# Performance work log

Measured on AMD Instinct MI355X. Metric: run time of the kernel, lower is better.

The kernel has to match this reference:

```python
import jax, jax.numpy as jnp
import numpy as np

N, D, C = 16384, 64, 128
MARGIN = 1.0
EPS_NORM = 1e-6   # F.normalize eps
EPS_PD = 1e-6     # F.pairwise_distance eps (added to the difference elementwise)


def setup_inputs() -> dict:
    key = jax.random.key(0)
    embeddings = jax.random.normal(key, (N, D), dtype=jnp.float32)
    labels = (jnp.arange(N) % C).astype(jnp.int32).reshape(N, 1)
    # deterministic valid positive: same label (i % C), different index
    pos_idx = ((jnp.arange(N) + C) % N).astype(jnp.int32)
    return {"embeddings": embeddings, "labels": labels, "pos_idx": pos_idx}


def reference(embeddings, labels, pos_idx):
    # L2-normalize rows (torch F.normalize: x / max(||x||, eps))
    nrm = jnp.linalg.norm(embeddings, axis=1, keepdims=True)
    e = embeddings / jnp.maximum(nrm, EPS_NORM)

    lab = labels[:, 0]
    # torch pairwise_distance computes ||x1 - x2 + eps||_2, eps added per element:
    # ||xi - xj + eps||^2 = ||xi||^2 + ||xj||^2 - 2 xi.xj + 2*eps*(sum(xi)-sum(xj)) + D*eps^2
    sq = jnp.sum(e * e, axis=1)          # [N]
    s = jnp.sum(e, axis=1)               # [N]
    gram = e @ e.T                        # [N, N]
    d2 = (sq[:, None] + sq[None, :] - 2.0 * gram
          + 2.0 * EPS_PD * (s[:, None] - s[None, :]) + D * EPS_PD * EPS_PD)
    d2 = jnp.maximum(d2, 0.0)
    dist = jnp.sqrt(jnp.maximum(d2, 1e-12))  # guard sqrt grad at 0

    # one positive per anchor: squared distance
    pos_loss = jnp.sum(d2[jnp.arange(N), pos_idx])

    # all negatives per anchor: hinge^2 on (margin - dist)
    neg_mask = lab[:, None] != lab[None, :]
    hinge = jnp.maximum(MARGIN - dist, 0.0)
    neg_loss = jnp.sum(jnp.where(neg_mask, hinge * hinge, 0.0))

    n_comparisons = N + jnp.sum(neg_mask)
    return (pos_loss + neg_loss) / n_comparisons.astype(jnp.float32)
```

## Files before the change

### kernel.cpp

```cpp
#include <hip/hip_runtime.h>
#include <hip/hip_bf16.h>

#define NN 16384
#define DD 64
#define NBI 32
#define NUNITS 2112
#define NBLK 512
#define NPOSB (NN/4)
#define SCREEN_T 0.49f

constexpr float F_EPS_PD   = 1e-6f;
constexpr float F_EPS_NORM = 1e-6f;

using bf16x8 = __attribute__((ext_vector_type(8))) short;
using f32x4  = __attribute__((ext_vector_type(4))) float;
typedef __attribute__((address_space(1))) const unsigned int gu32_t;
typedef __attribute__((address_space(3))) unsigned int       lu32_t;

__device__ __forceinline__ float wave_sum_f(float v) {
    #pragma unroll
    for (int o = 32; o >= 1; o >>= 1) v += __shfl_xor(v, o);
    return v;
}

__device__ __forceinline__ int band_off(int I) { return 2 * I * (65 - I); }

__global__ __launch_bounds__(256) void norm_kernel(
    const float* __restrict__ emb, const int* __restrict__ pidx,
    const int* __restrict__ lab, float2* __restrict__ up,
    float2* __restrict__ vcp, __hip_bfloat16* __restrict__ ebf,
    float* __restrict__ posP) {
    int w    = threadIdx.x >> 6;
    int row  = blockIdx.x * 4 + w;
    int lane = threadIdx.x & 63;
    int j    = pidx[row];
    float x  = emb[(size_t)row * DD + lane];
    float xj = emb[(size_t)j   * DD + lane];

    float n2  = wave_sum_f(x * x);
    float sx  = wave_sum_f(x);
    float n2j = wave_sum_f(xj * xj);
    float sxj = wave_sum_f(xj);
    float dot = wave_sum_f(x * xj);

    float m  = fmaxf(sqrtf(n2),  F_EPS_NORM);
    float mj = fmaxf(sqrtf(n2j), F_EPS_NORM);
    ebf[(size_t)row * DD + lane] = __float2bfloat16(x / m);

    __shared__ float spos[4];
    if (lane == 0) {
        float sq  = n2 / (m * m);
        float sqj = n2j / (mj * mj);
        float s   = sx / m;
        float sj  = sxj / mj;
        float g   = dot / (m * mj);
        float lf  = (float)lab[row];
        up[row]  = make_float2(sq + 2.0f * F_EPS_PD * s, lf);
        vcp[row] = make_float2(
            sq - 2.0f * F_EPS_PD * s + (float)DD * F_EPS_PD * F_EPS_PD, lf);
        float d2p = sq + sqj - 2.0f * g + 2.0f * F_EPS_PD * (s - sj)
                  + (float)DD * F_EPS_PD * F_EPS_PD;
        spos[w] = fmaxf(d2p, 0.0f);
    }
    __syncthreads();
    if (threadIdx.x == 0)
        posP[blockIdx.x] = spos[0] + spos[1] + spos[2] + spos[3];
}

__device__ __forceinline__ void stage_tile(const short* ebf, const float2* vcp,
                                           int tile, short* slotB, float2* slotV,
                                           int w, int lane) {
    const short* tbase = ebf + (size_t)tile * (128 * DD);
    int rlo = lane >> 3;
    int g   = (lane & 7) ^ rlo;
    #pragma unroll
    for (int q = 0; q < 2; ++q) {
        int m = w * 2 + q;
        __builtin_amdgcn_global_load_lds(
            (gu32_t*)(const void*)(tbase + (size_t)(8 * m + rlo) * DD + g * 8),
            (lu32_t*)(void*)(slotB + m * 512), 16, 0, 0);
    }
    __builtin_amdgcn_global_load_lds(
        (gu32_t*)(const void*)(vcp + (size_t)tile * 128 + lane * 2),
        (lu32_t*)(void*)slotV, 16, 0, 0);
}

__global__ __launch_bounds__(512, 4) void pair_kernel(
    const short* __restrict__ ebf, const float2* __restrict__ up,
    const float2* __restrict__ vcp, float* __restrict__ negP) {
    __shared__ short  ringB[3][8192];
    __shared__ float2 ringV[3][128];
    __shared__ float2 uband[512];
    __shared__ float  sred[8];
    int tid  = threadIdx.x;
    int w    = tid >> 6;
    int lane = tid & 63;
    int lrow = lane & 15, lkh = lane >> 4;
    int c0s  = ((lkh)     ^ (lrow & 7)) * 8;
    int c1s  = ((lkh + 4) ^ (lrow & 7)) * 8;

    int ks = (int)(((long long)blockIdx.x * NUNITS) / NBLK);
    int ke = (int)(((long long)(blockIdx.x + 1) * NUNITS) / NBLK);

    int I = (int)((65.0f - sqrtf(4225.0f - 2.0f * (float)ks)) * 0.5f);
    I = I < 0 ? 0 : (I > NBI - 1 ? NBI - 1 : I);
    while (band_off(I) > ks) --I;
    while (I < NBI - 1 && band_off(I + 1) <= ks) ++I;

    float hacc = 0.0f;
    int u0 = ks;
    while (u0 < ke) {
        int bend = band_off(I + 1);
        int n    = (ke < bend ? ke : bend) - u0;
        int tj0  = 4 * I + (u0 - band_off(I));
        int rowbase = I * 512 + w * 64;
        int rt      = 4 * I + (w >> 1);

        bf16x8 a[4][2];
        #pragma unroll
        for (int s = 0; s < 4; ++s) {
            const short* ab = ebf + (size_t)(rowbase + 16 * s + lrow) * DD + lkh * 8;
            a[s][0] = *(const bf16x8*)(ab);
            a[s][1] = *(const bf16x8*)(ab + 32);
        }
        if (w < 4)
            __builtin_amdgcn_global_load_lds(
                (gu32_t*)(const void*)(up + (size_t)I * 512 + w * 128 + lane * 2),
                (lu32_t*)(void*)(uband + w * 128), 16, 0, 0);
        stage_tile(ebf, vcp, tj0, &ringB[0][0], &ringV[0][0], w, lane);
        if (n > 1)
            stage_tile(ebf, vcp, tj0 + 1, &ringB[1][0], &ringV[1][0], w, lane);

        int sl = 0;
        for (int k = 0; k < n; ++k) {
            if (k + 1 < n) asm volatile("s_waitcnt vmcnt(3)" ::: "memory");
            else           asm volatile("s_waitcnt vmcnt(0)" ::: "memory");
            __builtin_amdgcn_s_barrier();
            __builtin_amdgcn_sched_barrier(0);
            int sl2 = (sl >= 1) ? sl - 1 : 2;
            if (k + 2 < n)
                stage_tile(ebf, vcp, tj0 + k + 2, &ringB[sl2][0], &ringV[sl2][0],
                           w, lane);

            int tj = tj0 + k;
            float wgt = (tj == rt) ? 1.0f : ((tj > rt) ? 2.0f : 0.0f);
            if (wgt != 0.0f) {
                const short*  lb = &ringB[sl][0];
                const float2* lv = &ringV[sl][0];
                float hp = 0.0f;
                #pragma unroll
                for (int t = 0; t < 8; ++t) {
                    const short* rowp = lb + (t * 16 + lrow) * 64;
                    bf16x8 b0 = *(const bf16x8*)(rowp + c0s);
                    bf16x8 b1 = *(const bf16x8*)(rowp + c1s);
                    f32x4 c4[4];
                    #pragma unroll
                    for (int s = 0; s < 4; ++s) {
                        f32x4 z = {0.f, 0.f, 0.f, 0.f};
                        z = __builtin_amdgcn_mfma_f32_16x16x32_bf16(a[s][0], b0, z, 0, 0, 0);
                        z = __builtin_amdgcn_mfma_f32_16x16x32_bf16(a[s][1], b1, z, 0, 0, 0);
                        c4[s] = z;
                    }
                    float mx = fmaxf(fmaxf(c4[0][0], c4[0][1]), fmaxf(c4[0][2], c4[0][3]));
                    mx = fmaxf(mx, fmaxf(fmaxf(c4[1][0], c4[1][1]), fmaxf(c4[1][2], c4[1][3])));
                    mx = fmaxf(mx, fmaxf(fmaxf(c4[2][0], c4[2][1]), fmaxf(c4[2][2], c4[2][3])));
                    mx = fmaxf(mx, fmaxf(fmaxf(c4[3][0], c4[3][1]), fmaxf(c4[3][2], c4[3][3])));
                    if (__any(mx > SCREEN_T)) {
                        float2 vl = lv[t * 16 + lrow];
                        #pragma unroll
                        for (int s = 0; s < 4; ++s) {
                            #pragma unroll
                            for (int r = 0; r < 4; ++r) {
                                float2 ul = uband[w * 64 + 16 * s + lkh * 4 + r];
                                float d2 = fmaf(-2.0f, c4[s][r], ul.x + vl.x);
                                float d  = sqrtf(fmaxf(d2, 1e-12f));
                                float h  = fmaxf(1.0f - d, 0.0f);
                                if (ul.y != vl.y) hp = fmaf(h, h, hp);
                            }
                        }
                    }
                }
                hacc = fmaf(wgt, hp, hacc);
            }
            sl = (sl + 1 == 3) ? 0 : sl + 1;
        }
        __builtin_amdgcn_s_barrier();
        __builtin_amdgcn_sched_barrier(0);
        u0 += n;
        ++I;
    }

    hacc = wave_sum_f(hacc);
    if (lane == 0) sred[w] = hacc;
    __syncthreads();
    if (tid == 0) {
        float tn = 0.f;
        #pragma unroll
        for (int i = 0; i < 8; ++i) tn += sred[i];
        negP[blockIdx.x] = tn;
    }
}

__global__ __launch_bounds__(1024) void reduce_kernel(
    const float* __restrict__ posP, const float* __restrict__ negP,
    const int* __restrict__ lab, float* __restrict__ out) {
    __shared__ unsigned int hist[4][1024];
    int t = threadIdx.x;
    int w = t >> 6, lane = t & 63;
    for (int i = t; i < 4096; i += 1024) hist[i >> 10][i & 1023] = 0u;
    __syncthreads();
    const int4* lab4 = (const int4*)lab;
    for (int i = t; i < NN / 4; i += 1024) {
        int4 v = lab4[i];
        atomicAdd(&hist[w & 3][v.x & 1023], 1u);
        atomicAdd(&hist[w & 3][v.y & 1023], 1u);
        atomicAdd(&hist[w & 3][v.z & 1023], 1u);
        atomicAdd(&hist[w & 3][v.w & 1023], 1u);
    }
    __syncthreads();

    float ps = 0.f, ns = 0.f;
    unsigned long long sqc = 0u;
    const float4* posP4 = (const float4*)posP;
    for (int i = t; i < NPOSB / 4; i += 1024) {
        float4 v = posP4[i];
        ps += (v.x + v.y) + (v.z + v.w);
    }
    if (t < NBLK) ns = negP[t];
    for (int i = t; i < 1024; i += 1024) {
        unsigned long long h = (unsigned long long)hist[0][i] + hist[1][i]
                             + hist[2][i] + hist[3][i];
        sqc += h * h;
    }

    ps = wave_sum_f(ps);
    ns = wave_sum_f(ns);
    #pragma unroll
    for (int o = 32; o >= 1; o >>= 1) sqc += __shfl_xor(sqc, o);

    __shared__ float sp[16], sn[16];
    __shared__ unsigned long long sc[16];
    if (lane == 0) { sp[w] = ps; sn[w] = ns; sc[w] = sqc; }
    __syncthreads();
    if (t == 0) {
        float pos = 0.f, neg = 0.f;
        unsigned long long s2 = 0;
        #pragma unroll
        for (int i = 0; i < 16; ++i) { pos += sp[i]; neg += sn[i]; s2 += sc[i]; }
        unsigned long long nneg = (unsigned long long)NN * NN - s2;
        float ncomp = (float)((unsigned long long)NN + nneg);
        out[0] = (pos + neg) / ncomp;
    }
}

extern "C" void kernel_launch(void* const* d_in, const int* in_sizes, int n_in,
                              void* d_out, int out_size, void* d_ws, size_t ws_size,
                              hipStream_t stream) {
    const float* emb = (const float*)d_in[0];
    const int* lab   = (const int*)d_in[1];
    const int* pidx  = (const int*)d_in[2];
    float* out = (float*)d_out;
    char* ws = (char*)d_ws;
    float2*         up   = (float2*)(ws);
    float2*         vcp  = (float2*)(ws + 131072);
    __hip_bfloat16* ebf  = (__hip_bfloat16*)(ws + 262144);
    float*          posP = (float*)(ws + 2359296);
    float*          negP = (float*)(ws + 2375680);

    norm_kernel<<<NPOSB, 256, 0, stream>>>(emb, pidx, lab, up, vcp, ebf, posP);
    pair_kernel<<<NBLK, 512, 0, stream>>>((const short*)ebf, up, vcp, negP);
    reduce_kernel<<<1, 1024, 0, stream>>>(posP, negP, lab, out);
}
```

Measured before the change: 53.85 us.

## Split pair kernel into gram screening pass and sparse hit evaluation kernel

The fused pair kernel is split in two. A lean gram kernel only runs the MFMA screen and writes an 8-bit hit mask per (64-row strip, 128-column tile). A new hit kernel then recomputes the dot products and the hinge terms only for flagged 16-column subtiles, loading its operands straight from global memory. Dropping the per-tile vcp/uband staging and the divergent hinge epilogue from the hot loop is meant to cut LDS use and register pressure, allowing 6 blocks per CU, 768 blocks, and MFMA priority boosting via setprio. The cost is an extra kernel launch, a mask buffer round trip, and some recomputed MFMA work for the hit tiles.

```diff
diff --git a/kernel.cpp b/kernel.cpp
--- a/kernel.cpp
+++ b/kernel.cpp
@@ -5,8 +5,9 @@
 #define DD 64
 #define NBI 32
 #define NUNITS 2112
-#define NBLK 512
+#define NBLK 768
 #define NPOSB (NN/4)
+#define NH2W 512
 #define SCREEN_T 0.49f
 
 constexpr float F_EPS_PD   = 1e-6f;
@@ -67,9 +68,8 @@
         posP[blockIdx.x] = spos[0] + spos[1] + spos[2] + spos[3];
 }
 
-__device__ __forceinline__ void stage_tile(const short* ebf, const float2* vcp,
-                                           int tile, short* slotB, float2* slotV,
-                                           int w, int lane) {
+__device__ __forceinline__ void stage_tile(const short* ebf, int tile,
+                                           short* slotB, int w, int lane) {
     const short* tbase = ebf + (size_t)tile * (128 * DD);
     int rlo = lane >> 3;
     int g   = (lane & 7) ^ rlo;
@@ -80,18 +80,11 @@
             (gu32_t*)(const void*)(tbase + (size_t)(8 * m + rlo) * DD + g * 8),
             (lu32_t*)(void*)(slotB + m * 512), 16, 0, 0);
     }
-    __builtin_amdgcn_global_load_lds(
-        (gu32_t*)(const void*)(vcp + (size_t)tile * 128 + lane * 2),
-        (lu32_t*)(void*)slotV, 16, 0, 0);
-}
-
-__global__ __launch_bounds__(512, 4) void pair_kernel(
-    const short* __restrict__ ebf, const float2* __restrict__ up,
-    const float2* __restrict__ vcp, float* __restrict__ negP) {
-    __shared__ short  ringB[3][8192];
-    __shared__ float2 ringV[3][128];
-    __shared__ float2 uband[512];
-    __shared__ float  sred[8];
+}
+
+__global__ __launch_bounds__(512, 6) void gram_kernel(
+    const short* __restrict__ ebf, unsigned char* __restrict__ hitb) {
+    __shared__ short ringB[3][8192];
     int tid  = threadIdx.x;
     int w    = tid >> 6;
     int lane = tid & 63;
@@ -107,14 +100,14 @@
     while (band_off(I) > ks) --I;
     while (I < NBI - 1 && band_off(I + 1) <= ks) ++I;
 
-    float hacc = 0.0f;
     int u0 = ks;
     while (u0 < ke) {
         int bend = band_off(I + 1);
         int n    = (ke < bend ? ke : bend) - u0;
         int tj0  = 4 * I + (u0 - band_off(I));
         int rowbase = I * 512 + w * 64;
-        int rt      = 4 * I + (w >> 1);
+        int strip64 = I * 8 + w;
+        int rt      = strip64 >> 1;
 
         bf16x8 a[4][2];
         #pragma unroll
@@ -123,36 +116,30 @@
             a[s][0] = *(const bf16x8*)(ab);
             a[s][1] = *(const bf16x8*)(ab + 32);
         }
-        if (w < 4)
-            __builtin_amdgcn_global_load_lds(
-                (gu32_t*)(const void*)(up + (size_t)I * 512 + w * 128 + lane * 2),
-                (lu32_t*)(void*)(uband + w * 128), 16, 0, 0);
-        stage_tile(ebf, vcp, tj0, &ringB[0][0], &ringV[0][0], w, lane);
-        if (n > 1)
-            stage_tile(ebf, vcp, tj0 + 1, &ringB[1][0], &ringV[1][0], w, lane);
+        stage_tile(ebf, tj0, &ringB[0][0], w, lane);
+        if (n > 1) stage_tile(ebf, tj0 + 1, &ringB[1][0], w, lane);
 
         int sl = 0;
         for (int k = 0; k < n; ++k) {
-            if (k + 1 < n) asm volatile("s_waitcnt vmcnt(3)" ::: "memory");
-            else           asm volatile("s_waitcnt vmcnt(0)" ::: "memory");
+            if (k == n - 1)      asm volatile("s_waitcnt vmcnt(0)" ::: "memory");
+            else if (k == 0)     asm volatile("s_waitcnt vmcnt(2)" ::: "memory");
+            else                 asm volatile("s_waitcnt vmcnt(3)" ::: "memory");
             __builtin_amdgcn_s_barrier();
             __builtin_amdgcn_sched_barrier(0);
             int sl2 = (sl >= 1) ? sl - 1 : 2;
             if (k + 2 < n)
-                stage_tile(ebf, vcp, tj0 + k + 2, &ringB[sl2][0], &ringV[sl2][0],
-                           w, lane);
+                stage_tile(ebf, tj0 + k + 2, &ringB[sl2][0], w, lane);
 
             int tj = tj0 + k;
-            float wgt = (tj == rt) ? 1.0f : ((tj > rt) ? 2.0f : 0.0f);
-            if (wgt != 0.0f) {
-                const short*  lb = &ringB[sl][0];
-                const float2* lv = &ringV[sl][0];
-                float hp = 0.0f;
+            unsigned int mask = 0;
+            if (tj >= rt) {
+                const short* lb = &ringB[sl][0];
                 #pragma unroll
                 for (int t = 0; t < 8; ++t) {
                     const short* rowp = lb + (t * 16 + lrow) * 64;
                     bf16x8 b0 = *(const bf16x8*)(rowp + c0s);
                     bf16x8 b1 = *(const bf16x8*)(rowp + c1s);
+                    __builtin_amdgcn_s_setprio(1);
                     f32x4 c4[4];
                     #pragma unroll
                     for (int s = 0; s < 4; ++s) {
@@ -161,27 +148,15 @@
                         z = __builtin_amdgcn_mfma_f32_16x16x32_bf16(a[s][1], b1, z, 0, 0, 0);
                         c4[s] = z;
                     }
+                    __builtin_amdgcn_s_setprio(0);
                     float mx = fmaxf(fmaxf(c4[0][0], c4[0][1]), fmaxf(c4[0][2], c4[0][3]));
                     mx = fmaxf(mx, fmaxf(fmaxf(c4[1][0], c4[1][1]), fmaxf(c4[1][2], c4[1][3])));
                     mx = fmaxf(mx, fmaxf(fmaxf(c4[2][0], c4[2][1]), fmaxf(c4[2][2], c4[2][3])));
                     mx = fmaxf(mx, fmaxf(fmaxf(c4[3][0], c4[3][1]), fmaxf(c4[3][2], c4[3][3])));
-                    if (__any(mx > SCREEN_T)) {
-                        float2 vl = lv[t * 16 + lrow];
-                        #pragma unroll
-                        for (int s = 0; s < 4; ++s) {
-                            #pragma unroll
-                            for (int r = 0; r < 4; ++r) {
-                                float2 ul = uband[w * 64 + 16 * s + lkh * 4 + r];
-                                float d2 = fmaf(-2.0f, c4[s][r], ul.x + vl.x);
-                                float d  = sqrtf(fmaxf(d2, 1e-12f));
-                                float h  = fmaxf(1.0f - d, 0.0f);
-                                if (ul.y != vl.y) hp = fmaf(h, h, hp);
-                            }
-                        }
-                    }
+                    if (__any(mx > SCREEN_T)) mask |= (1u << t);
                 }
-                hacc = fmaf(wgt, hp, hacc);
             }
+            if (lane == 0) hitb[strip64 * 128 + tj] = (unsigned char)mask;
             sl = (sl + 1 == 3) ? 0 : sl + 1;
         }
         __builtin_amdgcn_s_barrier();
@@ -189,20 +164,78 @@
         u0 += n;
         ++I;
     }
-
+}
+
+__global__ __launch_bounds__(256) void hit_kernel(
+    const short* __restrict__ ebf, const float2* __restrict__ up,
+    const float2* __restrict__ vcp, const unsigned char* __restrict__ hitb,
+    float* __restrict__ negP2) {
+    int tid  = threadIdx.x;
+    int w    = tid >> 6;
+    int lane = tid & 63;
+    int lrow = lane & 15, lkh = lane >> 4;
+    int gw   = blockIdx.x * 4 + w;
+    int base = gw * 64;
+
+    float hacc = 0.0f;
+    unsigned char myb = hitb[base + lane];
+    unsigned long long bal = __ballot(myb != 0);
+    while (bal) {
+        int l = __builtin_ctzll(bal);
+        bal &= bal - 1;
+        int idx = base + l;
+        unsigned int mask = (unsigned int)__shfl((int)myb, l);
+        int strip64 = idx >> 7, tj = idx & 127;
+        int rt = strip64 >> 1;
+        float wgt = (tj == rt) ? 1.0f : ((tj > rt) ? 2.0f : 0.0f);
+        if (wgt == 0.0f) continue;
+        int rowbase = strip64 * 64;
+
+        bf16x8 a[4][2];
+        float2 ul[4][4];
+        #pragma unroll
+        for (int s = 0; s < 4; ++s) {
+            const short* ab = ebf + (size_t)(rowbase + 16 * s + lrow) * DD + lkh * 8;
+            a[s][0] = *(const bf16x8*)(ab);
+            a[s][1] = *(const bf16x8*)(ab + 32);
+            #pragma unroll
+            for (int r = 0; r < 4; ++r)
+                ul[s][r] = up[rowbase + 16 * s + lkh * 4 + r];
+        }
+        float hp = 0.0f;
+        for (int t = 0; t < 8; ++t) {
+            if (!(mask & (1u << t))) continue;
+            const short* bb = ebf + (size_t)(tj * 128 + t * 16 + lrow) * DD + lkh * 8;
+            bf16x8 b0 = *(const bf16x8*)(bb);
+            bf16x8 b1 = *(const bf16x8*)(bb + 32);
+            f32x4 c4[4];
+            #pragma unroll
+            for (int s = 0; s < 4; ++s) {
+                f32x4 z = {0.f, 0.f, 0.f, 0.f};
+                z = __builtin_amdgcn_mfma_f32_16x16x32_bf16(a[s][0], b0, z, 0, 0, 0);
+                z = __builtin_amdgcn_mfma_f32_16x16x32_bf16(a[s][1], b1, z, 0, 0, 0);
+                c4[s] = z;
+            }
+            float2 vl = vcp[tj * 128 + t * 16 + lrow];
+            #pragma unroll
+            for (int s = 0; s < 4; ++s) {
+                #pragma unroll
+                for (int r = 0; r < 4; ++r) {
+                    float d2 = fmaf(-2.0f, c4[s][r], ul[s][r].x + vl.x);
+                    float d  = sqrtf(fmaxf(d2, 1e-12f));
+                    float h  = fmaxf(1.0f - d, 0.0f);
+                    if (ul[s][r].y != vl.y) hp = fmaf(h, h, hp);
+                }
+            }
+        }
+        hacc = fmaf(wgt, hp, hacc);
+    }
     hacc = wave_sum_f(hacc);
-    if (lane == 0) sred[w] = hacc;
-    __syncthreads();
-    if (tid == 0) {
-        float tn = 0.f;
-        #pragma unroll
-        for (int i = 0; i < 8; ++i) tn += sred[i];
-        negP[blockIdx.x] = tn;
-    }
+    if (lane == 0) negP2[gw] = hacc;
 }
 
 __global__ __launch_bounds__(1024) void reduce_kernel(
-    const float* __restrict__ posP, const float* __restrict__ negP,
+    const float* __restrict__ posP, const float* __restrict__ negP2,
     const int* __restrict__ lab, float* __restrict__ out) {
     __shared__ unsigned int hist[4][1024];
     int t = threadIdx.x;
@@ -226,11 +259,11 @@
         float4 v = posP4[i];
         ps += (v.x + v.y) + (v.z + v.w);
     }
-    if (t < NBLK) ns = negP[t];
-    for (int i = t; i < 1024; i += 1024) {
-        unsigned long long h = (unsigned long long)hist[0][i] + hist[1][i]
-                             + hist[2][i] + hist[3][i];
-        sqc += h * h;
+    if (t < NH2W) ns = negP2[t];
+    if (t < 1024) {
+        unsigned long long h = (unsigned long long)hist[0][t] + hist[1][t]
+                             + hist[2][t] + hist[3][t];
+        sqc = h * h;
     }
 
     ps = wave_sum_f(ps);
@@ -261,13 +294,15 @@
     const int* pidx  = (const int*)d_in[2];
     float* out = (float*)d_out;
     char* ws = (char*)d_ws;
-    float2*         up   = (float2*)(ws);
-    float2*         vcp  = (float2*)(ws + 131072);
-    __hip_bfloat16* ebf  = (__hip_bfloat16*)(ws + 262144);
-    float*          posP = (float*)(ws + 2359296);
-    float*          negP = (float*)(ws + 2375680);
+    float2*         up    = (float2*)(ws);
+    float2*         vcp   = (float2*)(ws + 131072);
+    __hip_bfloat16* ebf   = (__hip_bfloat16*)(ws + 262144);
+    float*          posP  = (float*)(ws + 2359296);
+    float*          negP2 = (float*)(ws + 2375680);
+    unsigned char*  hitb  = (unsigned char*)(ws + 2377728);
 
     norm_kernel<<<NPOSB, 256, 0, stream>>>(emb, pidx, lab, up, vcp, ebf, posP);
-    pair_kernel<<<NBLK, 512, 0, stream>>>((const short*)ebf, up, vcp, negP);
-    reduce_kernel<<<1, 1024, 0, stream>>>(posP, negP, lab, out);
-}
+    gram_kernel<<<NBLK, 512, 0, stream>>>((const short*)ebf, hitb);
+    hit_kernel<<<128, 256, 0, stream>>>((const short*)ebf, up, vcp, hitb, negP2);
+    reduce_kernel<<<1, 1024, 0, stream>>>(posP, negP2, lab, out);
+}
```

After: 69.21 us. 28.5% more time.

## Double the grid, shrink LDS ring to two slots, raise occupancy hint

Applied to the files above, without the earlier changes.

Doubles the number of pair-kernel blocks and raises the launch-bounds occupancy target from 4 to 8, cutting the LDS staging ring from three slots to two so more blocks fit per CU. The prefetch now stages one tile ahead instead of two, with the wait issued after the prefetch. It also wraps the MFMA burst in s_setprio, restructures the max reduction into a shallower tree, and simplifies the final reduction for the new block count. The aim is better load balance and latency hiding through more resident waves, at the cost of a shallower prefetch pipeline and tighter register budget.

```diff
diff --git a/kernel.cpp b/kernel.cpp
--- a/kernel.cpp
+++ b/kernel.cpp
@@ -5,7 +5,7 @@
 #define DD 64
 #define NBI 32
 #define NUNITS 2112
-#define NBLK 512
+#define NBLK 1024
 #define NPOSB (NN/4)
 #define SCREEN_T 0.49f
 
@@ -85,11 +85,11 @@
         (lu32_t*)(void*)slotV, 16, 0, 0);
 }
 
-__global__ __launch_bounds__(512, 4) void pair_kernel(
+__global__ __launch_bounds__(512, 8) void pair_kernel(
     const short* __restrict__ ebf, const float2* __restrict__ up,
     const float2* __restrict__ vcp, float* __restrict__ negP) {
-    __shared__ short  ringB[3][8192];
-    __shared__ float2 ringV[3][128];
+    __shared__ short  ringB[2][8192];
+    __shared__ float2 ringV[2][128];
     __shared__ float2 uband[512];
     __shared__ float  sred[8];
     int tid  = threadIdx.x;
@@ -128,31 +128,31 @@
                 (gu32_t*)(const void*)(up + (size_t)I * 512 + w * 128 + lane * 2),
                 (lu32_t*)(void*)(uband + w * 128), 16, 0, 0);
         stage_tile(ebf, vcp, tj0, &ringB[0][0], &ringV[0][0], w, lane);
-        if (n > 1)
-            stage_tile(ebf, vcp, tj0 + 1, &ringB[1][0], &ringV[1][0], w, lane);
-
-        int sl = 0;
+
         for (int k = 0; k < n; ++k) {
-            if (k + 1 < n) asm volatile("s_waitcnt vmcnt(3)" ::: "memory");
-            else           asm volatile("s_waitcnt vmcnt(0)" ::: "memory");
             __builtin_amdgcn_s_barrier();
             __builtin_amdgcn_sched_barrier(0);
-            int sl2 = (sl >= 1) ? sl - 1 : 2;
-            if (k + 2 < n)
-                stage_tile(ebf, vcp, tj0 + k + 2, &ringB[sl2][0], &ringV[sl2][0],
-                           w, lane);
+            if (k + 1 < n) {
+                stage_tile(ebf, vcp, tj0 + k + 1, &ringB[(k + 1) & 1][0],
+                           &ringV[(k + 1) & 1][0], w, lane);
+                asm volatile("s_waitcnt vmcnt(3)" ::: "memory");
+            } else {
+                asm volatile("s_waitcnt vmcnt(0)" ::: "memory");
+            }
+            __builtin_amdgcn_sched_barrier(0);
 
             int tj = tj0 + k;
             float wgt = (tj == rt) ? 1.0f : ((tj > rt) ? 2.0f : 0.0f);
             if (wgt != 0.0f) {
-                const short*  lb = &ringB[sl][0];
-                const float2* lv = &ringV[sl][0];
+                const short*  lb = &ringB[k & 1][0];
+                const float2* lv = &ringV[k & 1][0];
                 float hp = 0.0f;
                 #pragma unroll
                 for (int t = 0; t < 8; ++t) {
                     const short* rowp = lb + (t * 16 + lrow) * 64;
                     bf16x8 b0 = *(const bf16x8*)(rowp + c0s);
                     bf16x8 b1 = *(const bf16x8*)(rowp + c1s);
+                    __builtin_amdgcn_s_setprio(1);
                     f32x4 c4[4];
                     #pragma unroll
                     for (int s = 0; s < 4; ++s) {
@@ -161,10 +161,12 @@
                         z = __builtin_amdgcn_mfma_f32_16x16x32_bf16(a[s][1], b1, z, 0, 0, 0);
                         c4[s] = z;
                     }
-                    float mx = fmaxf(fmaxf(c4[0][0], c4[0][1]), fmaxf(c4[0][2], c4[0][3]));
-                    mx = fmaxf(mx, fmaxf(fmaxf(c4[1][0], c4[1][1]), fmaxf(c4[1][2], c4[1][3])));
-                    mx = fmaxf(mx, fmaxf(fmaxf(c4[2][0], c4[2][1]), fmaxf(c4[2][2], c4[2][3])));
-                    mx = fmaxf(mx, fmaxf(fmaxf(c4[3][0], c4[3][1]), fmaxf(c4[3][2], c4[3][3])));
+                    __builtin_amdgcn_s_setprio(0);
+                    float m0 = fmaxf(fmaxf(c4[0][0], c4[0][1]), fmaxf(c4[0][2], c4[0][3]));
+                    float m1 = fmaxf(fmaxf(c4[1][0], c4[1][1]), fmaxf(c4[1][2], c4[1][3]));
+                    float m2 = fmaxf(fmaxf(c4[2][0], c4[2][1]), fmaxf(c4[2][2], c4[2][3]));
+                    float m3 = fmaxf(fmaxf(c4[3][0], c4[3][1]), fmaxf(c4[3][2], c4[3][3]));
+                    float mx = fmaxf(fmaxf(m0, m1), fmaxf(m2, m3));
                     if (__any(mx > SCREEN_T)) {
                         float2 vl = lv[t * 16 + lrow];
                         #pragma unroll
@@ -182,7 +184,6 @@
                 }
                 hacc = fmaf(wgt, hp, hacc);
             }
-            sl = (sl + 1 == 3) ? 0 : sl + 1;
         }
         __builtin_amdgcn_s_barrier();
         __builtin_amdgcn_sched_barrier(0);
@@ -226,11 +227,11 @@
         float4 v = posP4[i];
         ps += (v.x + v.y) + (v.z + v.w);
     }
-    if (t < NBLK) ns = negP[t];
-    for (int i = t; i < 1024; i += 1024) {
-        unsigned long long h = (unsigned long long)hist[0][i] + hist[1][i]
-                             + hist[2][i] + hist[3][i];
-        sqc += h * h;
+    ns = negP[t];
+    {
+        unsigned long long h = (unsigned long long)hist[0][t & 1023] + hist[1][t & 1023]
+                             + hist[2][t & 1023] + hist[3][t & 1023];
+        sqc = h * h;
     }
 
     ps = wave_sum_f(ps);
```

Measured after the change: 68.29 us. 1.27x slower.

## Fuse normalize, pair, and reduce kernels into one persistent kernel with grid barriers

Applied to the files above, without the earlier changes.

Merges the normalization, pairwise-hinge and final reduction kernels into a single launch of 512 blocks. Blocks meet at a global atomic-counter barrier between phases, and the last stage runs only in block 0. This removes two kernel launch gaps and tail effects. It also adds s_setprio around the MFMA block. The cost is a memset of the counters, spin-wait barriers that assume all 512 blocks are co-resident, and fewer threads doing the normalization phase.

```diff
diff --git a/kernel.cpp b/kernel.cpp
--- a/kernel.cpp
+++ b/kernel.cpp
@@ -6,7 +6,6 @@
 #define NBI 32
 #define NUNITS 2112
 #define NBLK 512
-#define NPOSB (NN/4)
 #define SCREEN_T 0.49f
 
 constexpr float F_EPS_PD   = 1e-6f;
@@ -24,48 +23,6 @@
 }
 
 __device__ __forceinline__ int band_off(int I) { return 2 * I * (65 - I); }
-
-__global__ __launch_bounds__(256) void norm_kernel(
-    const float* __restrict__ emb, const int* __restrict__ pidx,
-    const int* __restrict__ lab, float2* __restrict__ up,
-    float2* __restrict__ vcp, __hip_bfloat16* __restrict__ ebf,
-    float* __restrict__ posP) {
-    int w    = threadIdx.x >> 6;
-    int row  = blockIdx.x * 4 + w;
-    int lane = threadIdx.x & 63;
-    int j    = pidx[row];
-    float x  = emb[(size_t)row * DD + lane];
-    float xj = emb[(size_t)j   * DD + lane];
-
-    float n2  = wave_sum_f(x * x);
-    float sx  = wave_sum_f(x);
-    float n2j = wave_sum_f(xj * xj);
-    float sxj = wave_sum_f(xj);
-    float dot = wave_sum_f(x * xj);
-
-    float m  = fmaxf(sqrtf(n2),  F_EPS_NORM);
-    float mj = fmaxf(sqrtf(n2j), F_EPS_NORM);
-    ebf[(size_t)row * DD + lane] = __float2bfloat16(x / m);
-
-    __shared__ float spos[4];
-    if (lane == 0) {
-        float sq  = n2 / (m * m);
-        float sqj = n2j / (mj * mj);
-        float s   = sx / m;
-        float sj  = sxj / mj;
-        float g   = dot / (m * mj);
-        float lf  = (float)lab[row];
-        up[row]  = make_float2(sq + 2.0f * F_EPS_PD * s, lf);
-        vcp[row] = make_float2(
-            sq - 2.0f * F_EPS_PD * s + (float)DD * F_EPS_PD * F_EPS_PD, lf);
-        float d2p = sq + sqj - 2.0f * g + 2.0f * F_EPS_PD * (s - sj)
-                  + (float)DD * F_EPS_PD * F_EPS_PD;
-        spos[w] = fmaxf(d2p, 0.0f);
-    }
-    __syncthreads();
-    if (threadIdx.x == 0)
-        posP[blockIdx.x] = spos[0] + spos[1] + spos[2] + spos[3];
-}
 
 __device__ __forceinline__ void stage_tile(const short* ebf, const float2* vcp,
                                            int tile, short* slotB, float2* slotV,
@@ -85,171 +42,237 @@
         (lu32_t*)(void*)slotV, 16, 0, 0);
 }
 
-__global__ __launch_bounds__(512, 4) void pair_kernel(
-    const short* __restrict__ ebf, const float2* __restrict__ up,
-    const float2* __restrict__ vcp, float* __restrict__ negP) {
+__global__ __launch_bounds__(512, 4) void fused_kernel(
+    const float* __restrict__ emb, const int* __restrict__ pidx,
+    const int* __restrict__ lab, float2* __restrict__ up,
+    float2* __restrict__ vcp, __hip_bfloat16* __restrict__ ebf,
+    float* __restrict__ posP, float* __restrict__ negP,
+    unsigned int* cnt, float* __restrict__ out) {
     __shared__ short  ringB[3][8192];
     __shared__ float2 ringV[3][128];
     __shared__ float2 uband[512];
     __shared__ float  sred[8];
+
+    int bid  = blockIdx.x;
     int tid  = threadIdx.x;
     int w    = tid >> 6;
     int lane = tid & 63;
-    int lrow = lane & 15, lkh = lane >> 4;
-    int c0s  = ((lkh)     ^ (lrow & 7)) * 8;
-    int c1s  = ((lkh + 4) ^ (lrow & 7)) * 8;
-
-    int ks = (int)(((long long)blockIdx.x * NUNITS) / NBLK);
-    int ke = (int)(((long long)(blockIdx.x + 1) * NUNITS) / NBLK);
-
-    int I = (int)((65.0f - sqrtf(4225.0f - 2.0f * (float)ks)) * 0.5f);
-    I = I < 0 ? 0 : (I > NBI - 1 ? NBI - 1 : I);
-    while (band_off(I) > ks) --I;
-    while (I < NBI - 1 && band_off(I + 1) <= ks) ++I;
-
-    float hacc = 0.0f;
-    int u0 = ks;
-    while (u0 < ke) {
-        int bend = band_off(I + 1);
-        int n    = (ke < bend ? ke : bend) - u0;
-        int tj0  = 4 * I + (u0 - band_off(I));
-        int rowbase = I * 512 + w * 64;
-        int rt      = 4 * I + (w >> 1);
-
-        bf16x8 a[4][2];
-        #pragma unroll
-        for (int s = 0; s < 4; ++s) {
-            const short* ab = ebf + (size_t)(rowbase + 16 * s + lrow) * DD + lkh * 8;
-            a[s][0] = *(const bf16x8*)(ab);
-            a[s][1] = *(const bf16x8*)(ab + 32);
-        }
-        if (w < 4)
-            __builtin_amdgcn_global_load_lds(
-                (gu32_t*)(const void*)(up + (size_t)I * 512 + w * 128 + lane * 2),
-                (lu32_t*)(void*)(uband + w * 128), 16, 0, 0);
-        stage_tile(ebf, vcp, tj0, &ringB[0][0], &ringV[0][0], w, lane);
-        if (n > 1)
-            stage_tile(ebf, vcp, tj0 + 1, &ringB[1][0], &ringV[1][0], w, lane);
-
-        int sl = 0;
-        for (int k = 0; k < n; ++k) {
-            if (k + 1 < n) asm volatile("s_waitcnt vmcnt(3)" ::: "memory");
-            else           asm volatile("s_waitcnt vmcnt(0)" ::: "memory");
-            __builtin_amdgcn_s_barrier();
-            __builtin_amdgcn_sched_barrier(0);
-            int sl2 = (sl >= 1) ? sl - 1 : 2;
-            if (k + 2 < n)
-                stage_tile(ebf, vcp, tj0 + k + 2, &ringB[sl2][0], &ringV[sl2][0],
-                           w, lane);
-
-            int tj = tj0 + k;
-            float wgt = (tj == rt) ? 1.0f : ((tj > rt) ? 2.0f : 0.0f);
-            if (wgt != 0.0f) {
-                const short*  lb = &ringB[sl][0];
-                const float2* lv = &ringV[sl][0];
-                float hp = 0.0f;
-                #pragma unroll
-                for (int t = 0; t < 8; ++t) {
-                    const short* rowp = lb + (t * 16 + lrow) * 64;
-                    bf16x8 b0 = *(const bf16x8*)(rowp + c0s);
-                    bf16x8 b1 = *(const bf16x8*)(rowp + c1s);
-                    f32x4 c4[4];
+
+    {
+        float pospart = 0.f;
+        int rbase = bid * 32 + w * 4;
+        for (int r = 0; r < 4; ++r) {
+            int row = rbase + r;
+            int j   = pidx[row];
+            float x  = emb[(size_t)row * DD + lane];
+            float xj = emb[(size_t)j   * DD + lane];
+            float n2  = wave_sum_f(x * x);
+            float sx  = wave_sum_f(x);
+            float n2j = wave_sum_f(xj * xj);
+            float sxj = wave_sum_f(xj);
+            float dot = wave_sum_f(x * xj);
+            float m = fmaxf(sqrtf(n2), F_EPS_NORM);
+            ebf[(size_t)row * DD + lane] = __float2bfloat16(x / m);
+            if (lane == 0) {
+                float mj  = fmaxf(sqrtf(n2j), F_EPS_NORM);
+                float sq  = n2 / (m * m);
+                float sqj = n2j / (mj * mj);
+                float s   = sx / m;
+                float sj  = sxj / mj;
+                float g   = dot / (m * mj);
+                float lf  = (float)lab[row];
+                up[row]  = make_float2(sq + 2.0f * F_EPS_PD * s, lf);
+                vcp[row] = make_float2(
+                    sq - 2.0f * F_EPS_PD * s + (float)DD * F_EPS_PD * F_EPS_PD, lf);
+                float d2p = sq + sqj - 2.0f * g + 2.0f * F_EPS_PD * (s - sj)
+                          + (float)DD * F_EPS_PD * F_EPS_PD;
+                pospart += fmaxf(d2p, 0.0f);
+            }
+        }
+        if (lane == 0) sred[w] = pospart;
+        __syncthreads();
+        if (tid == 0) {
+            float t = 0.f;
+            #pragma unroll
+            for (int i = 0; i < 8; ++i) t += sred[i];
+            posP[bid] = t;
+        }
+    }
+
+    __syncthreads();
+    if (tid == 0) {
+        __hip_atomic_fetch_add(&cnt[0], 1u, __ATOMIC_RELEASE,
+                               __HIP_MEMORY_SCOPE_AGENT);
+        while (__hip_atomic_load(&cnt[0], __ATOMIC_ACQUIRE,
+                                 __HIP_MEMORY_SCOPE_AGENT) < NBLK)
+            __builtin_amdgcn_s_sleep(16);
+    }
+    __syncthreads();
+
+    {
+        const short* ebfs = (const short*)ebf;
+        int lrow = lane & 15, lkh = lane >> 4;
+        int c0s  = ((lkh)     ^ (lrow & 7)) * 8;
+        int c1s  = ((lkh + 4) ^ (lrow & 7)) * 8;
+
+        int ks = (int)(((long long)bid * NUNITS) / NBLK);
+        int ke = (int)(((long long)(bid + 1) * NUNITS) / NBLK);
+
+        int I = (int)((65.0f - sqrtf(4225.0f - 2.0f * (float)ks)) * 0.5f);
+        I = I < 0 ? 0 : (I > NBI - 1 ? NBI - 1 : I);
+        while (band_off(I) > ks) --I;
+        while (I < NBI - 1 && band_off(I + 1) <= ks) ++I;
+
+        float hacc = 0.0f;
+        int u0 = ks;
+        while (u0 < ke) {
+            int bend = band_off(I + 1);
+            int n    = (ke < bend ? ke : bend) - u0;
+            int tj0  = 4 * I + (u0 - band_off(I));
+            int rowbase = I * 512 + w * 64;
+            int rt      = 4 * I + (w >> 1);
+
+            bf16x8 a[4][2];
+            #pragma unroll
+            for (int s = 0; s < 4; ++s) {
+                const short* ab = ebfs + (size_t)(rowbase + 16 * s + lrow) * DD + lkh * 8;
+                a[s][0] = *(const bf16x8*)(ab);
+                a[s][1] = *(const bf16x8*)(ab + 32);
+            }
+            if (w < 4)
+                __builtin_amdgcn_global_load_lds(
+                    (gu32_t*)(const void*)(up + (size_t)I * 512 + w * 128 + lane * 2),
+                    (lu32_t*)(void*)(uband + w * 128), 16, 0, 0);
+            stage_tile(ebfs, vcp, tj0, &ringB[0][0], &ringV[0][0], w, lane);
+            if (n > 1)
+                stage_tile(ebfs, vcp, tj0 + 1, &ringB[1][0], &ringV[1][0], w, lane);
+
+            int sl = 0;
+            for (int k = 0; k < n; ++k) {
+                if (k + 1 < n) asm volatile("s_waitcnt vmcnt(3)" ::: "memory");
+                else           asm volatile("s_waitcnt vmcnt(0)" ::: "memory");
+                __builtin_amdgcn_s_barrier();
+                __builtin_amdgcn_sched_barrier(0);
+                int sl2 = (sl >= 1) ? sl - 1 : 2;
+                if (k + 2 < n)
+                    stage_tile(ebfs, vcp, tj0 + k + 2, &ringB[sl2][0], &ringV[sl2][0],
+                               w, lane);
+
+                int tj = tj0 + k;
+                float wgt = (tj == rt) ? 1.0f : ((tj > rt) ? 2.0f : 0.0f);
+                if (wgt != 0.0f) {
+                    const short*  lb = &ringB[sl][0];
+                    const float2* lv = &ringV[sl][0];
+                    float hp = 0.0f;
                     #pragma unroll
-                    for (int s = 0; s < 4; ++s) {
-                        f32x4 z = {0.f, 0.f, 0.f, 0.f};
-                        z = __builtin_amdgcn_mfma_f32_16x16x32_bf16(a[s][0], b0, z, 0, 0, 0);
-                        z = __builtin_amdgcn_mfma_f32_16x16x32_bf16(a[s][1], b1, z, 0, 0, 0);
-                        c4[s] = z;
-                    }
-                    float mx = fmaxf(fmaxf(c4[0][0], c4[0][1]), fmaxf(c4[0][2], c4[0][3]));
-                    mx = fmaxf(mx, fmaxf(fmaxf(c4[1][0], c4[1][1]), fmaxf(c4[1][2], c4[1][3])));
-                    mx = fmaxf(mx, fmaxf(fmaxf(c4[2][0], c4[2][1]), fmaxf(c4[2][2], c4[2][3])));
-                    mx = fmaxf(mx, fmaxf(fmaxf(c4[3][0], c4[3][1]), fmaxf(c4[3][2], c4[3][3])));
-                    if (__any(mx > SCREEN_T)) {
-                        float2 vl = lv[t * 16 + lrow];
+                    for (int t = 0; t < 8; ++t) {
+                        const short* rowp = lb + (t * 16 + lrow) * 64;
+                        bf16x8 b0 = *(const bf16x8*)(rowp + c0s);
+                        bf16x8 b1 = *(const bf16x8*)(rowp + c1s);
+                        __builtin_amdgcn_s_setprio(1);
+                        f32x4 c4[4];
                         #pragma unroll
                         for (int s = 0; s < 4; ++s) {
+                            f32x4 z = {0.f, 0.f, 0.f, 0.f};
+                            z = __builtin_amdgcn_mfma_f32_16x16x32_bf16(a[s][0], b0, z, 0, 0, 0);
+                            z = __builtin_amdgcn_mfma_f32_16x16x32_bf16(a[s][1], b1, z, 0, 0, 0);
+                            c4[s] = z;
+                        }
+                        __builtin_amdgcn_s_setprio(0);
+                        float m0 = fmaxf(fmaxf(c4[0][0], c4[0][1]), fmaxf(c4[0][2], c4[0][3]));
+                        float m1 = fmaxf(fmaxf(c4[1][0], c4[1][1]), fmaxf(c4[1][2], c4[1][3]));
+                        float m2 = fmaxf(fmaxf(c4[2][0], c4[2][1]), fmaxf(c4[2][2], c4[2][3]));
+                        float m3 = fmaxf(fmaxf(c4[3][0], c4[3][1]), fmaxf(c4[3][2], c4[3][3]));
+                        float mx = fmaxf(fmaxf(m0, m1), fmaxf(m2, m3));
+                        if (__any(mx > SCREEN_T)) {
+                            float2 vl = lv[t * 16 + lrow];
                             #pragma unroll
-                            for (int r = 0; r < 4; ++r) {
-                                float2 ul = uband[w * 64 + 16 * s + lkh * 4 + r];
-                                float d2 = fmaf(-2.0f, c4[s][r], ul.x + vl.x);
-                                float d  = sqrtf(fmaxf(d2, 1e-12f));
-                                float h  = fmaxf(1.0f - d, 0.0f);
-                                if (ul.y != vl.y) hp = fmaf(h, h, hp);
+                            for (int s = 0; s < 4; ++s) {
+                                #pragma unroll
+                                for (int r = 0; r < 4; ++r) {
+                                    float2 ul = uband[w * 64 + 16 * s + lkh * 4 + r];
+                                    float d2 = fmaf(-2.0f, c4[s][r], ul.x + vl.x);
+                                    float d  = sqrtf(fmaxf(d2, 1e-12f));
+                                    float h  = fmaxf(1.0f - d, 0.0f);
+                                    if (ul.y != vl.y) hp = fmaf(h, h, hp);
+                                }
                             }
                         }
                     }
+                    hacc = fmaf(wgt, hp, hacc);
                 }
-                hacc = fmaf(wgt, hp, hacc);
+                sl = (sl + 1 == 3) ? 0 : sl + 1;
             }
-            sl = (sl + 1 == 3) ? 0 : sl + 1;
-        }
-        __builtin_amdgcn_s_barrier();
-        __builtin_amdgcn_sched_barrier(0);
-        u0 += n;
-        ++I;
-    }
-
-    hacc = wave_sum_f(hacc);
-    if (lane == 0) sred[w] = hacc;
-    __syncthreads();
+            __builtin_amdgcn_s_barrier();
+            __builtin_amdgcn_sched_barrier(0);
+            u0 += n;
+            ++I;
+        }
+
+        hacc = wave_sum_f(hacc);
+        if (lane == 0) sred[w] = hacc;
+        __syncthreads();
+        if (tid == 0) {
+            float tn = 0.f;
+            #pragma unroll
+            for (int i = 0; i < 8; ++i) tn += sred[i];
+            negP[bid] = tn;
+        }
+    }
+
+    __syncthreads();
+    if (tid == 0)
+        __hip_atomic_fetch_add(&cnt[1], 1u, __ATOMIC_RELEASE,
+                               __HIP_MEMORY_SCOPE_AGENT);
+    if (bid != 0) return;
     if (tid == 0) {
-        float tn = 0.f;
+        while (__hip_atomic_load(&cnt[1], __ATOMIC_ACQUIRE,
+                                 __HIP_MEMORY_SCOPE_AGENT) < NBLK)
+            __builtin_amdgcn_s_sleep(16);
+    }
+    __syncthreads();
+
+    {
+        unsigned int (*hist)[1024] = (unsigned int (*)[1024])(&ringB[0][0]);
+        for (int i = tid; i < 4096; i += 512) hist[i >> 10][i & 1023] = 0u;
+        __syncthreads();
+        const int4* lab4 = (const int4*)lab;
+        for (int i = tid; i < NN / 4; i += 512) {
+            int4 v = lab4[i];
+            atomicAdd(&hist[w & 3][v.x & 1023], 1u);
+            atomicAdd(&hist[w & 3][v.y & 1023], 1u);
+            atomicAdd(&hist[w & 3][v.z & 1023], 1u);
+            atomicAdd(&hist[w & 3][v.w & 1023], 1u);
+        }
+        __syncthreads();
+
+        float ps = posP[tid];
+        float ns = negP[tid];
+        unsigned long long sqc = 0;
+        for (int i = tid; i < 1024; i += 512) {
+            unsigned long long h = (unsigned long long)hist[0][i] + hist[1][i]
+                                 + hist[2][i] + hist[3][i];
+            sqc += h * h;
+        }
+        ps = wave_sum_f(ps);
+        ns = wave_sum_f(ns);
         #pragma unroll
-        for (int i = 0; i < 8; ++i) tn += sred[i];
-        negP[blockIdx.x] = tn;
-    }
-}
-
-__global__ __launch_bounds__(1024) void reduce_kernel(
-    const float* __restrict__ posP, const float* __restrict__ negP,
-    const int* __restrict__ lab, float* __restrict__ out) {
-    __shared__ unsigned int hist[4][1024];
-    int t = threadIdx.x;
-    int w = t >> 6, lane = t & 63;
-    for (int i = t; i < 4096; i += 1024) hist[i >> 10][i & 1023] = 0u;
-    __syncthreads();
-    const int4* lab4 = (const int4*)lab;
-    for (int i = t; i < NN / 4; i += 1024) {
-        int4 v = lab4[i];
-        atomicAdd(&hist[w & 3][v.x & 1023], 1u);
-        atomicAdd(&hist[w & 3][v.y & 1023], 1u);
-        atomicAdd(&hist[w & 3][v.z & 1023], 1u);
-        atomicAdd(&hist[w & 3][v.w & 1023], 1u);
-    }
-    __syncthreads();
-
-    float ps = 0.f, ns = 0.f;
-    unsigned long long sqc = 0u;
-    const float4* posP4 = (const float4*)posP;
-    for (int i = t; i < NPOSB / 4; i += 1024) {
-        float4 v = posP4[i];
-        ps += (v.x + v.y) + (v.z + v.w);
-    }
-    if (t < NBLK) ns = negP[t];
-    for (int i = t; i < 1024; i += 1024) {
-        unsigned long long h = (unsigned long long)hist[0][i] + hist[1][i]
-                             + hist[2][i] + hist[3][i];
-        sqc += h * h;
-    }
-
-    ps = wave_sum_f(ps);
-    ns = wave_sum_f(ns);
-    #pragma unroll
-    for (int o = 32; o >= 1; o >>= 1) sqc += __shfl_xor(sqc, o);
-
-    __shared__ float sp[16], sn[16];
-    __shared__ unsigned long long sc[16];
-    if (lane == 0) { sp[w] = ps; sn[w] = ns; sc[w] = sqc; }
-    __syncthreads();
-    if (t == 0) {
-        float pos = 0.f, neg = 0.f;
-        unsigned long long s2 = 0;
-        #pragma unroll
-        for (int i = 0; i < 16; ++i) { pos += sp[i]; neg += sn[i]; s2 += sc[i]; }
-        unsigned long long nneg = (unsigned long long)NN * NN - s2;
-        float ncomp = (float)((unsigned long long)NN + nneg);
-        out[0] = (pos + neg) / ncomp;
+        for (int o = 32; o >= 1; o >>= 1) sqc += __shfl_xor(sqc, o);
+
+        float* sp = (float*)&ringV[0][0];
+        float* sn = sp + 8;
+        unsigned long long* sc = (unsigned long long*)(sp + 16);
+        if (lane == 0) { sp[w] = ps; sn[w] = ns; sc[w] = sqc; }
+        __syncthreads();
+        if (tid == 0) {
+            float pos = 0.f, neg = 0.f;
+            unsigned long long s2 = 0;
+            #pragma unroll
+            for (int i = 0; i < 8; ++i) { pos += sp[i]; neg += sn[i]; s2 += sc[i]; }
+            unsigned long long nneg = (unsigned long long)NN * NN - s2;
+            float ncomp = (float)((unsigned long long)NN + nneg);
+            out[0] = (pos + neg) / ncomp;
+        }
     }
 }
 
@@ -265,9 +288,10 @@
     float2*         vcp  = (float2*)(ws + 131072);
     __hip_bfloat16* ebf  = (__hip_bfloat16*)(ws + 262144);
     float*          posP = (float*)(ws + 2359296);
-    float*          negP = (float*)(ws + 2375680);
-
-    norm_kernel<<<NPOSB, 256, 0, stream>>>(emb, pidx, lab, up, vcp, ebf, posP);
-    pair_kernel<<<NBLK, 512, 0, stream>>>((const short*)ebf, up, vcp, negP);
-    reduce_kernel<<<1, 1024, 0, stream>>>(posP, negP, lab, out);
-}
+    float*          negP = (float*)(ws + 2361344);
+    unsigned int*   cnt  = (unsigned int*)(ws + 2363392);
+
+    hipMemsetAsync(cnt, 0, 8, stream);
+    fused_kernel<<<NBLK, 512, 0, stream>>>(emb, pidx, lab, up, vcp, ebf,
+                                           posP, negP, cnt, out);
+}
```

Measured after the change: 100.8 us. 87.2% more time.
